# Optimization experiments

Measured on AMD Instinct MI355X. Metric: run time of the kernel, lower is better.

The kernel has to match this reference:

```python
import jax, jax.numpy as jnp
import numpy as np

B, T, E, H = 8, 1024, 1024, 16
D = E // H  # head_dim = 64


def setup_inputs() -> dict:
    key = jax.random.key(0)
    ks = jax.random.split(key, 11)
    s = 1.0 / np.sqrt(E)
    inp = {
        'query': jax.random.normal(ks[0], (B, T, E), jnp.float32),
        'key': jax.random.normal(ks[1], (B, T, E), jnp.float32),
        'value': jax.random.normal(ks[2], (B, T, E), jnp.float32),
        'Wq': jax.random.uniform(ks[3], (E, E), jnp.float32, -s, s),
        'bq': jax.random.uniform(ks[4], (E,), jnp.float32, -s, s),
        'Wk': jax.random.uniform(ks[5], (E, E), jnp.float32, -s, s),
        'bk': jax.random.uniform(ks[6], (E,), jnp.float32, -s, s),
        'Wv': jax.random.uniform(ks[7], (E, E), jnp.float32, -s, s),
        'bv': jax.random.uniform(ks[8], (E,), jnp.float32, -s, s),
        'Wo': jax.random.uniform(ks[9], (E, E), jnp.float32, -s, s),
        'bo': jax.random.uniform(ks[10], (E,), jnp.float32, -s, s),
    }
    return inp


def reference(query, key, value, Wq, bq, Wk, bk, Wv, bv, Wo, bo):
    scale = np.sqrt(D).astype(np.float32)
    # projections: Linear applies x @ W.T + b (torch convention); W shape (out,in)
    q = (query @ Wq.T + bq).reshape(B, T, H, D).transpose(0, 2, 1, 3)  # (B,H,Tq,D)
    k = (key @ Wk.T + bk).reshape(B, T, H, D).transpose(0, 2, 1, 3)    # (B,H,Tk,D)
    v = (value @ Wv.T + bv).reshape(B, T, H, D).transpose(0, 2, 1, 3)  # (B,H,Tk,D)
    scores = jnp.einsum('bhqd,bhkd->bhqk', q, k) / scale
    attn = jax.nn.softmax(scores, axis=-1)  # dropout = identity (eval)
    out = jnp.einsum('bhqk,bhkd->bhqd', attn, v)
    out = out.transpose(0, 2, 1, 3).reshape(B, T, E)
    return out @ Wo.T + bo
```

## Files before the change

### kernel.cpp

```cpp
#include <hip/hip_runtime.h>
#include <stdint.h>

#define BB 8
#define TT 1024
#define EE 1024
#define HH 16
#define DD 64

#define L2E8 0.18033688011112042f

typedef __attribute__((ext_vector_type(8))) __bf16 bf16x8;
typedef __attribute__((ext_vector_type(4))) float f32x4;
typedef __attribute__((ext_vector_type(4))) unsigned short ushort4v;
typedef __attribute__((ext_vector_type(4))) unsigned int uint4v;

__device__ __forceinline__ unsigned short f2bf(float f) {
  unsigned int u = __float_as_uint(f);
  u += 0x7fffu + ((u >> 16) & 1u);
  return (unsigned short)(u >> 16);
}

__device__ __forceinline__ unsigned int pk2t(float a, float b) {
  return __builtin_amdgcn_perm(__float_as_uint(b) + 0x8000u,
                               __float_as_uint(a) + 0x8000u, 0x07060302u);
}

__device__ __forceinline__ f32x4 mfma_16x16x32(bf16x8 a, bf16x8 b, f32x4 c) {
  return __builtin_amdgcn_mfma_f32_16x16x32_bf16(a, b, c, 0, 0, 0);
}

__device__ __forceinline__ void async_ld16(const unsigned short* g, unsigned short* l) {
  __builtin_amdgcn_global_load_lds(
      (const __attribute__((address_space(1))) void*)g,
      (__attribute__((address_space(3))) void*)l, 16, 0, 0);
}

__global__ __launch_bounds__(256) void cast_all(
    const float* __restrict__ xq, const float* __restrict__ xk, const float* __restrict__ xv,
    const float* __restrict__ wq, const float* __restrict__ wk,
    const float* __restrict__ wv, const float* __restrict__ wo,
    unsigned short* __restrict__ ws) {
  int blk = blockIdx.x;
  const float* src; size_t dstoff; int rel;
  if (blk < 4096)       { src = xq; dstoff = 0;        rel = blk; }
  else if (blk < 8192)  { src = xk; dstoff = 8388608;  rel = blk - 4096; }
  else if (blk < 12288) { src = xv; dstoff = 16777216; rel = blk - 8192; }
  else if (blk < 12800) { src = wq; dstoff = 25165824; rel = blk - 12288; }
  else if (blk < 13312) { src = wk; dstoff = 26214400; rel = blk - 12800; }
  else if (blk < 13824) { src = wv; dstoff = 27262976; rel = blk - 13312; }
  else                  { src = wo; dstoff = 28311552; rel = blk - 13824; }
  size_t base = (size_t)rel * 2048 + (size_t)threadIdx.x * 8;
  float4 a = *(const float4*)(src + base);
  float4 b = *(const float4*)(src + base + 4);
  ushort4v o0, o1;
  o0.x = f2bf(a.x); o0.y = f2bf(a.y); o0.z = f2bf(a.z); o0.w = f2bf(a.w);
  o1.x = f2bf(b.x); o1.y = f2bf(b.y); o1.z = f2bf(b.z); o1.w = f2bf(b.w);
  *(ushort4v*)(ws + dstoff + base) = o0;
  *(ushort4v*)(ws + dstoff + base + 4) = o1;
}

__global__ __launch_bounds__(256, 2) void fused_proj(
    const unsigned short* __restrict__ xq, const unsigned short* __restrict__ xk,
    const unsigned short* __restrict__ xv, const unsigned short* __restrict__ wq,
    const unsigned short* __restrict__ wk, const unsigned short* __restrict__ wv,
    const float* __restrict__ bq, const float* __restrict__ bk, const float* __restrict__ bv,
    unsigned short* __restrict__ Qb, unsigned short* __restrict__ Kb,
    unsigned short* __restrict__ Vtb) {
  const int id = blockIdx.x;
  const int tid = threadIdx.x;
  const int wave = tid >> 6, lane = tid & 63;
  const int quad = lane >> 4, l16 = lane & 15;
  const int wr = wave >> 1, wc = wave & 1;

  const unsigned short *A, *W;
  const float* bias;
  int mode, m0, n0;
  size_t zoff = 0;
  if (id < 512) {
    mode = 0; A = xq; W = wq; bias = bq;
    m0 = (id & 63) * 128; n0 = (id >> 6) * 128;
  } else if (id < 1024) {
    int t = id - 512;
    mode = 1; A = xk; W = wk; bias = bk;
    m0 = (t & 63) * 128; n0 = (t >> 6) * 128;
  } else {
    int t = id - 1024;
    int z = t >> 6;
    mode = 2; A = wv; W = xv + (size_t)z * 1048576; bias = bv;
    m0 = ((t >> 3) & 7) * 128; n0 = (t & 7) * 128;
    zoff = (size_t)z * 1048576;
  }

  __shared__ __align__(16) unsigned short As[2][128 * 64];
  __shared__ __align__(16) unsigned short Bs[2][128 * 64];

  const unsigned short* Wb = W + (size_t)n0 * 1024;

  f32x4 acc[4][4];
#pragma unroll
  for (int i = 0; i < 4; ++i)
#pragma unroll
    for (int j = 0; j < 4; ++j) acc[i][j] = (f32x4){0.f, 0.f, 0.f, 0.f};

  const int row_s = tid >> 3, c_s = tid & 7;
  const int swl = l16 & 7;

  auto stage = [&](int sel, int kt) {
    const unsigned short* Akt = A + (size_t)m0 * 1024 + kt * 64;
    const unsigned short* Wkt = Wb + kt * 64;
#pragma unroll
    for (int i = 0; i < 4; ++i) {
      int g = i * 256 + tid;
      int row = row_s + i * 32;
      int gc = c_s ^ (row & 7);
      async_ld16(Akt + (size_t)row * 1024 + gc * 8, &As[sel][g * 8]);
      async_ld16(Wkt + (size_t)row * 1024 + gc * 8, &Bs[sel][g * 8]);
    }
  };

  stage(0, 0);
  stage(1, 1);
  asm volatile("s_waitcnt vmcnt(8)" ::: "memory");
  __builtin_amdgcn_s_barrier();

  for (int kt = 0; kt < 16; ++kt) {
    const int cur = kt & 1;
#pragma unroll
    for (int ks = 0; ks < 2; ++ks) {
      bf16x8 af[4], bfv[4];
      const int sc = (ks * 4 + quad) ^ swl;
#pragma unroll
      for (int i = 0; i < 4; ++i)
        af[i] = *(const bf16x8*)(&As[cur][((wr * 64 + i * 16 + l16) * 8 + sc) * 8]);
#pragma unroll
      for (int j = 0; j < 4; ++j)
        bfv[j] = *(const bf16x8*)(&Bs[cur][((wc * 64 + j * 16 + l16) * 8 + sc) * 8]);
      __builtin_amdgcn_s_setprio(1);
#pragma unroll
      for (int i = 0; i < 4; ++i)
#pragma unroll
        for (int j = 0; j < 4; ++j) acc[i][j] = mfma_16x16x32(af[i], bfv[j], acc[i][j]);
      __builtin_amdgcn_s_setprio(0);
    }
    __builtin_amdgcn_s_barrier();
    int ktc = kt + 2 > 15 ? 15 : kt + 2;
    stage(cur, ktc);
    asm volatile("s_waitcnt vmcnt(8)" ::: "memory");
    __builtin_amdgcn_s_barrier();
  }

  if (mode == 2) {
    size_t base = zoff;
    const int nxor = ((((l16 >> 2) + 1) & 2) ? 12 : 0);
#pragma unroll
    for (int i = 0; i < 4; ++i)
#pragma unroll
      for (int r = 0; r < 4; ++r) {
        int m = m0 + wr * 64 + i * 16 + quad * 4 + r;
        float bm = bias[m];
#pragma unroll
        for (int j = 0; j < 4; ++j) {
          int n = (n0 + wc * 64 + j * 16 + l16) ^ nxor;
          Vtb[base + (size_t)m * 1024 + n] = f2bf(acc[i][j][r] + bm);
        }
      }
  } else {
    unsigned short* Out = (mode == 0) ? Qb : Kb;
    const float scale = (mode == 0) ? L2E8 : 1.0f;
#pragma unroll
    for (int j = 0; j < 4; ++j) {
      int n = n0 + wc * 64 + j * 16 + l16;
      float bn = bias[n];
      int h = n >> 6, d = n & 63;
#pragma unroll
      for (int i = 0; i < 4; ++i)
#pragma unroll
        for (int r = 0; r < 4; ++r) {
          int m = m0 + wr * 64 + i * 16 + quad * 4 + r;
          int b = m >> 10, t = m & 1023;
          float v = (acc[i][j][r] + bn) * scale;
          Out[((size_t)((b << 4) + h) * 1024 + t) * 64 + d] = f2bf(v);
        }
    }
  }
}

__global__ __launch_bounds__(256, 3) void gemm_out(
    const unsigned short* __restrict__ A, const unsigned short* __restrict__ Wm,
    const float* __restrict__ bias, float* __restrict__ Cout) {
  const int tid = threadIdx.x;
  const int wave = tid >> 6, lane = tid & 63;
  const int quad = lane >> 4, l16 = lane & 15;
  const int wr = wave >> 1, wc = wave & 1;
  const int m0 = blockIdx.x * 64;
  const int n0 = blockIdx.y * 128;

  __shared__ __align__(16) unsigned short As[2][64 * 64];
  __shared__ __align__(16) unsigned short Bs[2][128 * 64];

  const unsigned short* Wb = Wm + (size_t)n0 * 1024;

  f32x4 acc[2][4];
#pragma unroll
  for (int i = 0; i < 2; ++i)
#pragma unroll
    for (int j = 0; j < 4; ++j) acc[i][j] = (f32x4){0.f, 0.f, 0.f, 0.f};

  const int row_s = tid >> 3, c_s = tid & 7;
  const int swl = l16 & 7;

  auto stage = [&](int sel, int kt) {
    const unsigned short* Akt =
        A + (size_t)(m0 >> 10) * 1048576 + (size_t)kt * 65536 + (size_t)(m0 & 1023) * 64;
    const unsigned short* Wkt = Wb + kt * 64;
#pragma unroll
    for (int i = 0; i < 2; ++i) {
      int row = row_s + i * 32;
      int gc = c_s ^ (row & 7);
      async_ld16(Akt + (size_t)row * 64 + gc * 8, &As[sel][(i * 256 + tid) * 8]);
    }
#pragma unroll
    for (int i = 0; i < 4; ++i) {
      int row = row_s + i * 32;
      int gc = c_s ^ (row & 7);
      async_ld16(Wkt + (size_t)row * 1024 + gc * 8, &Bs[sel][(i * 256 + tid) * 8]);
    }
  };

  stage(0, 0);
  stage(1, 1);
  asm volatile("s_waitcnt vmcnt(6)" ::: "memory");
  __builtin_amdgcn_s_barrier();

  for (int kt = 0; kt < 16; ++kt) {
    const int cur = kt & 1;
#pragma unroll
    for (int ks = 0; ks < 2; ++ks) {
      bf16x8 af[2], bfv[4];
      const int sc = (ks * 4 + quad) ^ swl;
#pragma unroll
      for (int i = 0; i < 2; ++i)
        af[i] = *(const bf16x8*)(&As[cur][((wr * 32 + i * 16 + l16) * 8 + sc) * 8]);
#pragma unroll
      for (int j = 0; j < 4; ++j)
        bfv[j] = *(const bf16x8*)(&Bs[cur][((wc * 64 + j * 16 + l16) * 8 + sc) * 8]);
      __builtin_amdgcn_s_setprio(1);
#pragma unroll
      for (int i = 0; i < 2; ++i)
#pragma unroll
        for (int j = 0; j < 4; ++j) acc[i][j] = mfma_16x16x32(af[i], bfv[j], acc[i][j]);
      __builtin_amdgcn_s_setprio(0);
    }
    __builtin_amdgcn_s_barrier();
    int ktc = kt + 2 > 15 ? 15 : kt + 2;
    stage(cur, ktc);
    asm volatile("s_waitcnt vmcnt(6)" ::: "memory");
    __builtin_amdgcn_s_barrier();
  }

#pragma unroll
  for (int j = 0; j < 4; ++j) {
    int n = n0 + wc * 64 + j * 16 + l16;
    float bn = bias[n];
#pragma unroll
    for (int i = 0; i < 2; ++i)
#pragma unroll
      for (int r = 0; r < 4; ++r) {
        int m = m0 + wr * 32 + i * 16 + quad * 4 + r;
        Cout[(size_t)m * 1024 + n] = acc[i][j][r] + bn;
      }
  }
}

__global__ __launch_bounds__(256) void attn(
    const unsigned short* __restrict__ Q,
    const unsigned short* __restrict__ K,
    const unsigned short* __restrict__ Vt,
    unsigned short* __restrict__ O) {
  const int bh = blockIdx.x;
  const int tid = threadIdx.x;
  const int wave = tid >> 6, lane = tid & 63;
  const int quad = lane >> 4, l16 = lane & 15;
  const int q0 = blockIdx.y * 128 + wave * 32;
  const size_t bhTD = (size_t)bh * (TT * DD);
  const unsigned short* Qb = Q + bhTD;
  const unsigned short* Kb = K + bhTD;
  const unsigned short* Vb = Vt + bhTD;

  __shared__ __align__(16) unsigned short Ks[64 * 64];
  __shared__ __align__(16) unsigned short Vs[64 * 64];

  bf16x8 q_lo[2], q_hi[2];
#pragma unroll
  for (int g = 0; g < 2; ++g) {
    q_lo[g] = *(const bf16x8*)(Qb + (size_t)(q0 + g * 16 + l16) * 64 + quad * 8);
    q_hi[g] = *(const bf16x8*)(Qb + (size_t)(q0 + g * 16 + l16) * 64 + 32 + quad * 8);
  }

  uint4v ou; ou.x = ou.y = ou.z = ou.w = 0x3F803F80u;
  const bf16x8 ones = __builtin_bit_cast(bf16x8, ou);

  f32x4 o_acc[2][4];
#pragma unroll
  for (int g = 0; g < 2; ++g)
#pragma unroll
    for (int dd = 0; dd < 4; ++dd) o_acc[g][dd] = (f32x4){0.f, 0.f, 0.f, 0.f};
  f32x4 acc5[2];
  acc5[0] = (f32x4){0.f, 0.f, 0.f, 0.f};
  acc5[1] = (f32x4){0.f, 0.f, 0.f, 0.f};
  const bool lo_half = (quad < 2);

  const int srow = tid >> 3;
  const int schunk = tid & 7;

  for (int it = 0; it < 16; ++it) {
    const int kv0 = it * 64;
#pragma unroll
    for (int i = 0; i < 2; ++i) {
      int row = srow + i * 32;
      int gc = schunk ^ (row & 7);
      async_ld16(Kb + (size_t)(kv0 + row) * 64 + gc * 8, Ks + (row * 8 + schunk) * 8);
      async_ld16(Vb + (size_t)row * 1024 + kv0 + gc * 8, Vs + (row * 8 + schunk) * 8);
    }
    __syncthreads();

    f32x4 f[2][4];
#pragma unroll
    for (int c = 0; c < 2; ++c) {
      const int r0 = c * 32 + l16;
      const int r1 = r0 + 16;
      const int sw = r0 & 7;
      bf16x8 k00 = *(const bf16x8*)(Ks + (r0 * 8 + (quad ^ sw)) * 8);
      bf16x8 k01 = *(const bf16x8*)(Ks + (r0 * 8 + ((quad + 4) ^ sw)) * 8);
      bf16x8 k10 = *(const bf16x8*)(Ks + (r1 * 8 + (quad ^ sw)) * 8);
      bf16x8 k11 = *(const bf16x8*)(Ks + (r1 * 8 + ((quad + 4) ^ sw)) * 8);
      __builtin_amdgcn_s_setprio(1);
#pragma unroll
      for (int g = 0; g < 2; ++g) {
        f32x4 a = (f32x4){0.f, 0.f, 0.f, 0.f};
        f32x4 b = (f32x4){0.f, 0.f, 0.f, 0.f};
        a = mfma_16x16x32(k00, q_lo[g], a);
        a = mfma_16x16x32(k01, q_hi[g], a);
        b = mfma_16x16x32(k10, q_lo[g], b);
        b = mfma_16x16x32(k11, q_hi[g], b);
        f[g][2 * c] = a; f[g][2 * c + 1] = b;
      }
      __builtin_amdgcn_s_setprio(0);
    }

#pragma unroll
    for (int c = 0; c < 2; ++c) {
      bf16x8 ap[2];
#pragma unroll
      for (int g = 0; g < 2; ++g) {
        f32x4 f0 = f[g][2 * c], f1 = f[g][2 * c + 1];
        float p0 = __builtin_amdgcn_exp2f(f0[0]), p1 = __builtin_amdgcn_exp2f(f0[1]);
        float p2 = __builtin_amdgcn_exp2f(f0[2]), p3 = __builtin_amdgcn_exp2f(f0[3]);
        float p4 = __builtin_amdgcn_exp2f(f1[0]), p5 = __builtin_amdgcn_exp2f(f1[1]);
        float p6 = __builtin_amdgcn_exp2f(f1[2]), p7 = __builtin_amdgcn_exp2f(f1[3]);
        unsigned int u01 = pk2t(p0, p1), u23 = pk2t(p2, p3);
        unsigned int u45 = pk2t(p4, p5), u67 = pk2t(p6, p7);
        unsigned int pu01 = __shfl_xor(u01, 32), pu23 = __shfl_xor(u23, 32);
        unsigned int pu45 = __shfl_xor(u45, 32), pu67 = __shfl_xor(u67, 32);
        uint4v av;
        av.x = lo_half ? u01 : pu45;
        av.y = lo_half ? u23 : pu67;
        av.z = lo_half ? pu01 : u45;
        av.w = lo_half ? pu23 : u67;
        ap[g] = __builtin_bit_cast(bf16x8, av);
        acc5[g] = mfma_16x16x32(ap[g], ones, acc5[g]);
      }
      __builtin_amdgcn_s_setprio(1);
#pragma unroll
      for (int dd = 0; dd < 4; ++dd) {
        int vr = dd * 16 + l16;
        bf16x8 bv = *(const bf16x8*)(Vs + (vr * 8 + ((c * 4 + quad) ^ (vr & 7))) * 8);
#pragma unroll
        for (int g = 0; g < 2; ++g)
          o_acc[g][dd] = mfma_16x16x32(ap[g], bv, o_acc[g][dd]);
      }
      __builtin_amdgcn_s_setprio(0);
    }
    __syncthreads();
  }
#pragma unroll
  for (int g = 0; g < 2; ++g)
#pragma unroll
    for (int r = 0; r < 4; ++r) {
      float invr = 1.f / acc5[g][r];
      int trow = q0 + g * 16 + quad * 4 + r;
#pragma unroll
      for (int dd = 0; dd < 4; ++dd)
        O[bhTD + (size_t)trow * 64 + dd * 16 + l16] = f2bf(o_acc[g][dd][r] * invr);
    }
}

extern "C" void kernel_launch(void* const* d_in, const int* in_sizes, int n_in,
                              void* d_out, int out_size, void* d_ws, size_t ws_size,
                              hipStream_t stream) {
  const float* xq = (const float*)d_in[0];
  const float* xk = (const float*)d_in[1];
  const float* xv = (const float*)d_in[2];
  const float* Wq = (const float*)d_in[3];
  const float* bq = (const float*)d_in[4];
  const float* Wk = (const float*)d_in[5];
  const float* bk = (const float*)d_in[6];
  const float* Wv = (const float*)d_in[7];
  const float* bv = (const float*)d_in[8];
  const float* Wo = (const float*)d_in[9];
  const float* bo = (const float*)d_in[10];

  unsigned short* ws = (unsigned short*)d_ws;
  unsigned short* xq_b = ws;
  unsigned short* xk_b = ws + 8388608;
  unsigned short* xv_b = ws + 16777216;
  unsigned short* wq_b = ws + 25165824;
  unsigned short* wk_b = ws + 26214400;
  unsigned short* wv_b = ws + 27262976;
  unsigned short* wo_b = ws + 28311552;
  unsigned short* Qbuf = ws + 29360128;
  unsigned short* Kbuf = ws + 37748736;
  unsigned short* Vtb  = ws + 46137344;
  unsigned short* Obuf = ws + 54525952;

  cast_all<<<14336, 256, 0, stream>>>(xq, xk, xv, Wq, Wk, Wv, Wo, ws);

  fused_proj<<<1536, 256, 0, stream>>>(xq_b, xk_b, xv_b, wq_b, wk_b, wv_b,
                                       bq, bk, bv, Qbuf, Kbuf, Vtb);
  attn<<<dim3(128, 8), 256, 0, stream>>>(Qbuf, Kbuf, Vtb, Obuf);
  gemm_out<<<dim3(128, 8), 256, 0, stream>>>(Obuf, wo_b, bo, (float*)d_out);
}
```

Measured before the change: 314.7 us.

## Enlarge projection GEMM tiles to 256x256 with 8 waves and phased staging

After: 333.2 us. 1.06x slower.

```diff
diff --git a/kernel.cpp b/kernel.cpp
--- a/kernel.cpp
+++ b/kernel.cpp
@@ -59,7 +59,7 @@
   *(ushort4v*)(ws + dstoff + base + 4) = o1;
 }
 
-__global__ __launch_bounds__(256, 2) void fused_proj(
+__global__ __launch_bounds__(512, 2) void fused_proj(
     const unsigned short* __restrict__ xq, const unsigned short* __restrict__ xk,
     const unsigned short* __restrict__ xv, const unsigned short* __restrict__ wq,
     const unsigned short* __restrict__ wk, const unsigned short* __restrict__ wv,
@@ -70,118 +70,144 @@
   const int tid = threadIdx.x;
   const int wave = tid >> 6, lane = tid & 63;
   const int quad = lane >> 4, l16 = lane & 15;
-  const int wr = wave >> 1, wc = wave & 1;
+  const int wr = (wave >> 2) & 1, wc = wave & 3;
 
   const unsigned short *A, *W;
   const float* bias;
   int mode, m0, n0;
   size_t zoff = 0;
-  if (id < 512) {
+  if (id < 128) {
     mode = 0; A = xq; W = wq; bias = bq;
-    m0 = (id & 63) * 128; n0 = (id >> 6) * 128;
-  } else if (id < 1024) {
-    int t = id - 512;
+    m0 = (id & 31) * 256; n0 = (id >> 5) * 256;
+  } else if (id < 256) {
+    int t = id - 128;
     mode = 1; A = xk; W = wk; bias = bk;
-    m0 = (t & 63) * 128; n0 = (t >> 6) * 128;
+    m0 = (t & 31) * 256; n0 = (t >> 5) * 256;
   } else {
-    int t = id - 1024;
-    int z = t >> 6;
+    int t = id - 256;
+    int z = t & 7;
     mode = 2; A = wv; W = xv + (size_t)z * 1048576; bias = bv;
-    m0 = ((t >> 3) & 7) * 128; n0 = (t & 7) * 128;
+    m0 = (t >> 5) * 256; n0 = ((t >> 3) & 3) * 256;
     zoff = (size_t)z * 1048576;
   }
 
-  __shared__ __align__(16) unsigned short As[2][128 * 64];
-  __shared__ __align__(16) unsigned short Bs[2][128 * 64];
+  __shared__ __align__(16) unsigned short As[2][256 * 64];
+  __shared__ __align__(16) unsigned short Bs[2][256 * 64];
 
   const unsigned short* Wb = W + (size_t)n0 * 1024;
 
-  f32x4 acc[4][4];
-#pragma unroll
-  for (int i = 0; i < 4; ++i)
-#pragma unroll
-    for (int j = 0; j < 4; ++j) acc[i][j] = (f32x4){0.f, 0.f, 0.f, 0.f};
+  f32x4 acc[2][4][2][2];
+#pragma unroll
+  for (int mh = 0; mh < 2; ++mh)
+#pragma unroll
+    for (int i = 0; i < 4; ++i)
+#pragma unroll
+      for (int nh = 0; nh < 2; ++nh)
+#pragma unroll
+        for (int j = 0; j < 2; ++j) acc[mh][i][nh][j] = (f32x4){0.f, 0.f, 0.f, 0.f};
 
   const int row_s = tid >> 3, c_s = tid & 7;
   const int swl = l16 & 7;
 
-  auto stage = [&](int sel, int kt) {
-    const unsigned short* Akt = A + (size_t)m0 * 1024 + kt * 64;
-    const unsigned short* Wkt = Wb + kt * 64;
-#pragma unroll
-    for (int i = 0; i < 4; ++i) {
-      int g = i * 256 + tid;
-      int row = row_s + i * 32;
-      int gc = c_s ^ (row & 7);
-      async_ld16(Akt + (size_t)row * 1024 + gc * 8, &As[sel][g * 8]);
-      async_ld16(Wkt + (size_t)row * 1024 + gc * 8, &Bs[sel][g * 8]);
+  auto stageA = [&](int sel, int kt, int h) {
+    const unsigned short* src = A + (size_t)(m0 + h * 128) * 1024 + kt * 64;
+#pragma unroll
+    for (int i = 0; i < 2; ++i) {
+      int rr = row_s + i * 64;
+      int gc = c_s ^ (rr & 7);
+      async_ld16(src + (size_t)rr * 1024 + gc * 8, &As[sel][((h * 128 + rr) * 8 + c_s) * 8]);
     }
   };
-
-  stage(0, 0);
-  stage(1, 1);
-  asm volatile("s_waitcnt vmcnt(8)" ::: "memory");
-  __builtin_amdgcn_s_barrier();
-
-  for (int kt = 0; kt < 16; ++kt) {
-    const int cur = kt & 1;
-#pragma unroll
-    for (int ks = 0; ks < 2; ++ks) {
-      bf16x8 af[4], bfv[4];
-      const int sc = (ks * 4 + quad) ^ swl;
+  auto stageB = [&](int sel, int kt, int h) {
+    const unsigned short* src = Wb + (size_t)(h * 128) * 1024 + kt * 64;
+#pragma unroll
+    for (int i = 0; i < 2; ++i) {
+      int rr = row_s + i * 64;
+      int gc = c_s ^ (rr & 7);
+      async_ld16(src + (size_t)rr * 1024 + gc * 8, &Bs[sel][((h * 128 + rr) * 8 + c_s) * 8]);
+    }
+  };
+
+#define PROJ_PHASE(MH, NH, STG)                                                     \
+  {                                                                                 \
+    bf16x8 af[4][2], bf[2][2];                                                      \
+    _Pragma("unroll") for (int i = 0; i < 4; ++i) {                                 \
+      int row = MH * 128 + wr * 64 + i * 16 + l16;                                  \
+      _Pragma("unroll") for (int ks = 0; ks < 2; ++ks)                              \
+        af[i][ks] = *(const bf16x8*)(&As[slot][(row * 8 + ((ks * 4 + quad) ^ swl)) * 8]); \
+    }                                                                               \
+    _Pragma("unroll") for (int j = 0; j < 2; ++j) {                                 \
+      int row = NH * 128 + wc * 32 + j * 16 + l16;                                  \
+      _Pragma("unroll") for (int ks = 0; ks < 2; ++ks)                              \
+        bf[j][ks] = *(const bf16x8*)(&Bs[slot][(row * 8 + ((ks * 4 + quad) ^ swl)) * 8]); \
+    }                                                                               \
+    STG;                                                                            \
+    __builtin_amdgcn_s_barrier();                                                   \
+    __builtin_amdgcn_s_setprio(1);                                                  \
+    _Pragma("unroll") for (int ks = 0; ks < 2; ++ks)                                \
+      _Pragma("unroll") for (int i = 0; i < 4; ++i)                                 \
+        _Pragma("unroll") for (int j = 0; j < 2; ++j)                               \
+          acc[MH][i][NH][j] = mfma_16x16x32(af[i][ks], bf[j][ks], acc[MH][i][NH][j]); \
+    __builtin_amdgcn_s_setprio(0);                                                  \
+    __builtin_amdgcn_s_barrier();                                                   \
+  }
+
+  stageA(0, 0, 0); stageB(0, 0, 0); stageA(0, 0, 1); stageB(0, 0, 1);
+  stageA(1, 1, 0); stageB(1, 1, 0);
+
+  for (int t = 0; t < 16; ++t) {
+    const int slot = t & 1, nslot = slot ^ 1;
+    const int t1 = (t + 1 > 15) ? 15 : t + 1;
+    const int t2 = (t + 2 > 15) ? 15 : t + 2;
+    asm volatile("s_waitcnt vmcnt(4)" ::: "memory");
+    __builtin_amdgcn_s_barrier();
+    PROJ_PHASE(0, 0, stageA(nslot, t1, 1));
+    PROJ_PHASE(0, 1, stageB(nslot, t1, 1));
+    PROJ_PHASE(1, 0, stageA(slot, t2, 0));
+    PROJ_PHASE(1, 1, stageB(slot, t2, 0));
+  }
+#undef PROJ_PHASE
+
+  if (mode == 2) {
+    const int nxor = ((((l16 >> 2) + 1) & 2) ? 12 : 0);
+#pragma unroll
+    for (int mh = 0; mh < 2; ++mh)
 #pragma unroll
       for (int i = 0; i < 4; ++i)
-        af[i] = *(const bf16x8*)(&As[cur][((wr * 64 + i * 16 + l16) * 8 + sc) * 8]);
-#pragma unroll
-      for (int j = 0; j < 4; ++j)
-        bfv[j] = *(const bf16x8*)(&Bs[cur][((wc * 64 + j * 16 + l16) * 8 + sc) * 8]);
-      __builtin_amdgcn_s_setprio(1);
-#pragma unroll
-      for (int i = 0; i < 4; ++i)
-#pragma unroll
-        for (int j = 0; j < 4; ++j) acc[i][j] = mfma_16x16x32(af[i], bfv[j], acc[i][j]);
-      __builtin_amdgcn_s_setprio(0);
-    }
-    __builtin_amdgcn_s_barrier();
-    int ktc = kt + 2 > 15 ? 15 : kt + 2;
-    stage(cur, ktc);
-    asm volatile("s_waitcnt vmcnt(8)" ::: "memory");
-    __builtin_amdgcn_s_barrier();
-  }
-
-  if (mode == 2) {
-    size_t base = zoff;
-    const int nxor = ((((l16 >> 2) + 1) & 2) ? 12 : 0);
-#pragma unroll
-    for (int i = 0; i < 4; ++i)
-#pragma unroll
-      for (int r = 0; r < 4; ++r) {
-        int m = m0 + wr * 64 + i * 16 + quad * 4 + r;
-        float bm = bias[m];
-#pragma unroll
-        for (int j = 0; j < 4; ++j) {
-          int n = (n0 + wc * 64 + j * 16 + l16) ^ nxor;
-          Vtb[base + (size_t)m * 1024 + n] = f2bf(acc[i][j][r] + bm);
+#pragma unroll
+        for (int r = 0; r < 4; ++r) {
+          int m = m0 + mh * 128 + wr * 64 + i * 16 + quad * 4 + r;
+          float bm = bias[m];
+#pragma unroll
+          for (int nh = 0; nh < 2; ++nh)
+#pragma unroll
+            for (int j = 0; j < 2; ++j) {
+              int n = (n0 + nh * 128 + wc * 32 + j * 16 + l16) ^ nxor;
+              Vtb[zoff + (size_t)m * 1024 + n] = f2bf(acc[mh][i][nh][j][r] + bm);
+            }
         }
-      }
   } else {
     unsigned short* Out = (mode == 0) ? Qb : Kb;
     const float scale = (mode == 0) ? L2E8 : 1.0f;
 #pragma unroll
-    for (int j = 0; j < 4; ++j) {
-      int n = n0 + wc * 64 + j * 16 + l16;
-      float bn = bias[n];
-      int h = n >> 6, d = n & 63;
-#pragma unroll
-      for (int i = 0; i < 4; ++i)
-#pragma unroll
-        for (int r = 0; r < 4; ++r) {
-          int m = m0 + wr * 64 + i * 16 + quad * 4 + r;
-          int b = m >> 10, t = m & 1023;
-          float v = (acc[i][j][r] + bn) * scale;
-          Out[((size_t)((b << 4) + h) * 1024 + t) * 64 + d] = f2bf(v);
-        }
-    }
+    for (int nh = 0; nh < 2; ++nh)
+#pragma unroll
+      for (int j = 0; j < 2; ++j) {
+        int n = n0 + nh * 128 + wc * 32 + j * 16 + l16;
+        float bn = bias[n];
+        int h = n >> 6, d = n & 63;
+#pragma unroll
+        for (int mh = 0; mh < 2; ++mh)
+#pragma unroll
+          for (int i = 0; i < 4; ++i)
+#pragma unroll
+            for (int r = 0; r < 4; ++r) {
+              int m = m0 + mh * 128 + wr * 64 + i * 16 + quad * 4 + r;
+              int b = m >> 10, tt = m & 1023;
+              float v = (acc[mh][i][nh][j][r] + bn) * scale;
+              Out[((size_t)((b << 4) + h) * 1024 + tt) * 64 + d] = f2bf(v);
+            }
+      }
   }
 }
 
@@ -425,8 +451,8 @@
 
   cast_all<<<14336, 256, 0, stream>>>(xq, xk, xv, Wq, Wk, Wv, Wo, ws);
 
-  fused_proj<<<1536, 256, 0, stream>>>(xq_b, xk_b, xv_b, wq_b, wk_b, wv_b,
-                                       bq, bk, bv, Qbuf, Kbuf, Vtb);
+  fused_proj<<<384, 512, 0, stream>>>(xq_b, xk_b, xv_b, wq_b, wk_b, wv_b,
+                                      bq, bk, bv, Qbuf, Kbuf, Vtb);
   attn<<<dim3(128, 8), 256, 0, stream>>>(Qbuf, Kbuf, Vtb, Obuf);
   gemm_out<<<dim3(128, 8), 256, 0, stream>>>(Obuf, wo_b, bo, (float*)d_out);
 }
```
